# Performance work log

Measured on AMD Instinct MI355X. Metric: run time of the kernel, lower is better.

Reference implementation:

```python
import jax, jax.numpy as jnp
import numpy as np

N = 50000    # nodes
E = 800000   # edges (avg degree 16)
IN = 256     # in_dim
HID = 256    # hidden_dim
OUT = 128    # out_dim


def setup_inputs() -> dict:
    key = jax.random.key(0)
    ks = jax.random.split(key, 9)
    features = jax.random.normal(ks[0], (N, IN), jnp.float32)
    src = jax.random.randint(ks[1], (E,), 0, N, jnp.int32)
    dst = jax.random.randint(ks[2], (E,), 0, N, jnp.int32)
    noise = jax.random.normal(ks[3], (N, OUT), jnp.float32)
    def glorot(k, shape, fan):
        return jax.random.normal(k, shape, jnp.float32) / np.float32(np.sqrt(fan))
    W1 = glorot(ks[4], (IN, HID), IN);  b1 = jnp.zeros((HID,), jnp.float32)
    W2 = glorot(ks[5], (HID, OUT), HID); b2 = jnp.zeros((OUT,), jnp.float32)
    W3 = glorot(ks[6], (HID, OUT), HID); b3 = jnp.zeros((OUT,), jnp.float32)
    fcW = glorot(ks[7], (HID, IN), IN)   # nn.Linear(in_dim, hidden_dim).weight: [HID, IN]
    return dict(features=features, noise=noise, W1=W1, b1=b1, W2=W2, b2=b2,
                W3=W3, b3=b3, fcW=fcW, src=src, dst=dst)


def _gcn(x, W, b, src, dst, out_norm, in_norm):
    """DGL GraphConv norm='both': D_out^{-1/2} A D_in^{-1/2} X W + b."""
    x = x * out_norm[:, None]          # scale src features by out-deg^{-1/2}
    x = x @ W                          # dense transform (order commutes with SpMM)
    agg = jax.ops.segment_sum(x[src], dst, num_segments=N)  # sparse aggregate
    return agg * in_norm[:, None] + b


def reference(features, noise, W1, b1, W2, b2, W3, b3, fcW, src, dst):
    ones = jnp.ones((E,), jnp.float32)
    out_deg = jax.ops.segment_sum(ones, src, num_segments=N)
    in_deg = jax.ops.segment_sum(ones, dst, num_segments=N)
    out_norm = jnp.maximum(out_deg, 1.0) ** -0.5
    in_norm = jnp.maximum(in_deg, 1.0) ** -0.5

    h = jax.nn.relu(_gcn(features, W1, b1, src, dst, out_norm, in_norm))
    mean = jax.nn.relu(_gcn(h, W2, b2, src, dst, out_norm, in_norm))
    log_std = _gcn(h, W3, b3, src, dst, out_norm, in_norm)  # identity activation
    z = mean + noise * jnp.exp(log_std)
    seq_fts = features @ fcW.T
    return z, h, seq_fts
```

## Files before the change

kernel.cpp:

```cpp
#include <hip/hip_runtime.h>
#include <hip/hip_bf16.h>
#include <stdint.h>
#include <math.h>

#define IN_DIM 256
#define HID_DIM 256
#define OUT_DIM 128

typedef __attribute__((ext_vector_type(8))) short short8;
typedef __attribute__((ext_vector_type(4))) float floatx4;

__device__ __forceinline__ float bf2f(ushort u) {
  union { uint32_t i; float f; } v; v.i = ((uint32_t)u) << 16; return v.f;
}
__device__ __forceinline__ ushort f2bf(float f) {
  union { float f; uint32_t u; } v; v.f = f;
  uint32_t u = v.u;
  uint32_t r = u + 0x7fffu + ((u >> 16) & 1u);
  return (ushort)(r >> 16);
}

__global__ void f2b_kernel(const float* __restrict__ in, ushort* __restrict__ out, int n) {
  int base = (blockIdx.x * 256 + threadIdx.x) * 4;
  if (base < n) {
    float4 v = *(const float4*)(in + base);
    ushort4 o;
    o.x = f2bf(v.x); o.y = f2bf(v.y); o.z = f2bf(v.z); o.w = f2bf(v.w);
    *(ushort4*)(out + base) = o;
  }
}

__global__ void deg_kernel(const int* __restrict__ src, const int* __restrict__ dst,
                           int* __restrict__ out_deg, int* __restrict__ in_deg, int E) {
  int e = blockIdx.x * 256 + threadIdx.x;
  if (e < E) {
    atomicAdd(&out_deg[src[e]], 1);
    atomicAdd(&in_deg[dst[e]], 1);
  }
}

__global__ void scan_sums(const int* __restrict__ deg, int* __restrict__ chunk_sum, int n) {
  __shared__ int lds[256];
  int b = blockIdx.x, t = threadIdx.x;
  int base = b * 1024 + t * 4;
  int s = 0;
  if (base + 3 < n) {
    int4 v = *(const int4*)(deg + base);
    s = v.x + v.y + v.z + v.w;
  } else {
    for (int i = 0; i < 4; ++i) if (base + i < n) s += deg[base + i];
  }
  lds[t] = s;
  __syncthreads();
  for (int off = 128; off > 0; off >>= 1) {
    if (t < off) lds[t] += lds[t + off];
    __syncthreads();
  }
  if (t == 0) chunk_sum[b] = lds[0];
}

__global__ void scan_chunks(const int* __restrict__ chunk_sum, int* __restrict__ chunk_off,
                            int nchunks, int* __restrict__ row_ptr) {
  __shared__ int lds[256];
  int t = threadIdx.x;
  int v = (t < nchunks) ? chunk_sum[t] : 0;
  lds[t] = v;
  __syncthreads();
  for (int off = 1; off < 256; off <<= 1) {
    int add = (t >= off) ? lds[t - off] : 0;
    __syncthreads();
    lds[t] += add;
    __syncthreads();
  }
  if (t < nchunks) chunk_off[t] = lds[t] - v;
  if (t == 0) row_ptr[0] = 0;
}

__global__ void scan_final(const int* __restrict__ deg, const int* __restrict__ chunk_off,
                           int* __restrict__ row_ptr, int n) {
  __shared__ int lds[256];
  int b = blockIdx.x, t = threadIdx.x;
  int base = b * 1024 + t * 4;
  int v[4]; int s = 0;
#pragma unroll
  for (int i = 0; i < 4; ++i) { v[i] = (base + i < n) ? deg[base + i] : 0; s += v[i]; }
  lds[t] = s;
  __syncthreads();
  for (int off = 1; off < 256; off <<= 1) {
    int add = (t >= off) ? lds[t - off] : 0;
    __syncthreads();
    lds[t] += add;
    __syncthreads();
  }
  int run = lds[t] - s + chunk_off[b];
#pragma unroll
  for (int i = 0; i < 4; ++i) {
    run += v[i];
    if (base + i < n) row_ptr[base + i + 1] = run;
  }
}

__global__ void fill_kernel(const int* __restrict__ src, const int* __restrict__ dst,
                            const int* __restrict__ row_ptr, int* __restrict__ fill_cnt,
                            const int* __restrict__ out_deg,
                            int* __restrict__ edge_src, float* __restrict__ edge_w, int E) {
  int e = blockIdx.x * 256 + threadIdx.x;
  if (e < E) {
    int d = dst[e];
    int s = src[e];
    int pos = row_ptr[d] + atomicAdd(&fill_cnt[d], 1);
    int od = out_deg[s]; if (od < 1) od = 1;
    edge_src[pos] = s;
    edge_w[pos] = rsqrtf((float)od);
  }
}

__global__ void prep_weights(const float* __restrict__ W1, const float* __restrict__ W2,
                             const float* __restrict__ W3, const float* __restrict__ b2,
                             const float* __restrict__ b3, const float* __restrict__ fcW,
                             ushort* __restrict__ W1T, ushort* __restrict__ WcT,
                             float* __restrict__ bcat, ushort* __restrict__ fcWb) {
  int k = blockIdx.x;
  int n = threadIdx.x;
  W1T[n * 256 + k] = f2bf(W1[k * 256 + n]);
  WcT[n * 256 + k] = f2bf((n < 128) ? W2[k * 128 + n] : W3[k * 128 + (n - 128)]);
  fcWb[k * 256 + n] = f2bf(fcW[k * 256 + n]);
  if (k == 0) bcat[n] = (n < 128) ? b2[n] : b3[n - 128];
}

__global__ __launch_bounds__(256) void agg_kernel(
    const ushort* __restrict__ x, const int* __restrict__ row_ptr,
    const int* __restrict__ edge_src, const float* __restrict__ edge_w,
    const int* __restrict__ in_deg, ushort* __restrict__ out, int N) {
  int wave = threadIdx.x >> 6, lane = threadIdx.x & 63;
  int n = blockIdx.x * 4 + wave;
  if (n >= N) return;
  int half = lane >> 5;
  int hl = lane & 31;
  int start = row_ptr[n], end = row_ptr[n + 1];
  float acc[8];
#pragma unroll
  for (int k = 0; k < 8; ++k) acc[k] = 0.f;

  for (int base = start; base < end; base += 4) {
    int i0 = base + half;
    int i1 = base + 2 + half;
    int s0 = 0, s1 = 0; float w0 = 0.f, w1 = 0.f;
    if (i0 < end) { s0 = edge_src[i0]; w0 = edge_w[i0]; }
    if (i1 < end) { s1 = edge_src[i1]; w1 = edge_w[i1]; }
    uint4 v0 = *(const uint4*)&x[(size_t)s0 * 256 + hl * 8];
    uint4 v1 = *(const uint4*)&x[(size_t)s1 * 256 + hl * 8];
    const uint32_t* p0 = (const uint32_t*)&v0;
    const uint32_t* p1 = (const uint32_t*)&v1;
#pragma unroll
    for (int k = 0; k < 4; ++k) {
      acc[2 * k]     += bf2f((ushort)(p0[k] & 0xffffu)) * w0;
      acc[2 * k + 1] += bf2f((ushort)(p0[k] >> 16)) * w0;
      acc[2 * k]     += bf2f((ushort)(p1[k] & 0xffffu)) * w1;
      acc[2 * k + 1] += bf2f((ushort)(p1[k] >> 16)) * w1;
    }
  }
#pragma unroll
  for (int k = 0; k < 8; ++k) acc[k] += __shfl_xor(acc[k], 32, 64);

  if (half == 0) {
    int id = in_deg[n]; if (id < 1) id = 1;
    float inn = rsqrtf((float)id);
    uint4 o;
    uint32_t* po = (uint32_t*)&o;
#pragma unroll
    for (int k = 0; k < 4; ++k) {
      po[k] = ((uint32_t)f2bf(acc[2 * k + 1] * inn) << 16) |
              (uint32_t)f2bf(acc[2 * k] * inn);
    }
    *(uint4*)&out[(size_t)n * 256 + hl * 8] = o;
  }
}

__global__ __launch_bounds__(256, 2) void gemm_kernel(
    const ushort* __restrict__ A, const ushort* __restrict__ BT,
    const float* __restrict__ bias, const float* __restrict__ noise,
    float* __restrict__ C32, ushort* __restrict__ Cbf, int M, int mode) {
  __shared__ alignas(16) ushort A_lds[128 * 72];
  __shared__ alignas(16) ushort B_lds[256 * 72];
  int t = threadIdx.x;
  int m0 = blockIdx.x * 128;
  int wave = t >> 6, lane = t & 63;
  int wm = wave * 32;
  int l15 = lane & 15, quad = lane >> 4;

  floatx4 acc[2][16];
#pragma unroll
  for (int i = 0; i < 2; ++i)
#pragma unroll
    for (int j = 0; j < 16; ++j) acc[i][j] = (floatx4)(0.f);

  for (int kc = 0; kc < 256; kc += 64) {
#pragma unroll
    for (int r = 0; r < 4; ++r) {
      int idx = t + r * 256;
      int row = idx >> 3;
      int c = (idx & 7) << 3;
      int grow = m0 + row; if (grow > M - 1) grow = M - 1;
      *(uint4*)&A_lds[row * 72 + c] = *(const uint4*)(A + (size_t)grow * 256 + kc + c);
    }
#pragma unroll
    for (int r = 0; r < 8; ++r) {
      int idx = t + r * 256;
      int row = idx >> 3;
      int c = (idx & 7) << 3;
      *(uint4*)&B_lds[row * 72 + c] = *(const uint4*)(BT + (size_t)row * 256 + kc + c);
    }
    __syncthreads();
#pragma unroll
    for (int ko = 0; ko < 2; ++ko) {
      short8 a[2];
#pragma unroll
      for (int i = 0; i < 2; ++i)
        a[i] = *(const short8*)&A_lds[(wm + i * 16 + l15) * 72 + ko * 32 + quad * 8];
#pragma unroll
      for (int j = 0; j < 16; ++j) {
        short8 b = *(const short8*)&B_lds[(j * 16 + l15) * 72 + ko * 32 + quad * 8];
#pragma unroll
        for (int i = 0; i < 2; ++i)
          acc[i][j] = __builtin_amdgcn_mfma_f32_16x16x32_bf16(a[i], b, acc[i][j], 0, 0, 0);
      }
    }
    __syncthreads();
  }

  if (mode == 1) {
#pragma unroll
    for (int i = 0; i < 2; ++i) {
#pragma unroll
      for (int j = 0; j < 8; ++j) {
        int col = j * 16 + l15;
        float bm = bias[col];
        float bl = bias[col + 128];
#pragma unroll
        for (int r = 0; r < 4; ++r) {
          int row = m0 + wm + i * 16 + quad * 4 + r;
          if (row < M) {
            float mean = acc[i][j][r] + bm;
            float ls = acc[i][j + 8][r] + bl;
            size_t o = (size_t)row * 128 + col;
            C32[o] = fmaxf(mean, 0.f) + noise[o] * expf(ls);
          }
        }
      }
    }
  } else {
#pragma unroll
    for (int i = 0; i < 2; ++i) {
#pragma unroll
      for (int j = 0; j < 16; ++j) {
        int col = j * 16 + l15;
        float bv = (mode == 0) ? bias[col] : 0.f;
#pragma unroll
        for (int r = 0; r < 4; ++r) {
          int row = m0 + wm + i * 16 + quad * 4 + r;
          if (row < M) {
            float v = acc[i][j][r] + bv;
            if (mode == 0) v = fmaxf(v, 0.f);
            size_t o = (size_t)row * 256 + col;
            C32[o] = v;
            if (mode == 0) Cbf[o] = f2bf(v);
          }
        }
      }
    }
  }
}

extern "C" void kernel_launch(void* const* d_in, const int* in_sizes, int n_in,
                              void* d_out, int out_size, void* d_ws, size_t ws_size,
                              hipStream_t stream) {
  const float* features = (const float*)d_in[0];
  const float* noise    = (const float*)d_in[1];
  const float* W1 = (const float*)d_in[2];
  const float* b1 = (const float*)d_in[3];
  const float* W2 = (const float*)d_in[4];
  const float* b2 = (const float*)d_in[5];
  const float* W3 = (const float*)d_in[6];
  const float* b3 = (const float*)d_in[7];
  const float* fcW = (const float*)d_in[8];
  const int* src = (const int*)d_in[9];
  const int* dst = (const int*)d_in[10];
  const int N = in_sizes[0] / IN_DIM;
  const int E = in_sizes[9];

  float* out = (float*)d_out;
  float* z_out = out;
  float* h_out = out + (size_t)N * OUT_DIM;
  float* s_out = h_out + (size_t)N * HID_DIM;

  char* w = (char*)d_ws;
  auto carve = [&](size_t bytes) {
    char* p = w;
    w += (bytes + 255) & ~(size_t)255;
    return p;
  };
  ushort* feat_bf = (ushort*)carve((size_t)N * 256 * 2);
  ushort* h_bf    = (ushort*)carve((size_t)N * 256 * 2);
  ushort* agg_buf = (ushort*)carve((size_t)N * 256 * 2);
  ushort* W1T  = (ushort*)carve(256 * 256 * 2);
  ushort* WcT  = (ushort*)carve(256 * 256 * 2);
  ushort* fcWb = (ushort*)carve(256 * 256 * 2);
  float*  bcat = (float*)carve(256 * 4);
  int* degs    = (int*)carve((size_t)3 * N * 4);
  int* out_deg = degs;
  int* in_deg  = degs + N;
  int* fill_cnt = degs + 2 * N;
  int* row_ptr  = (int*)carve((size_t)(N + 1) * 4);
  int* edge_src = (int*)carve((size_t)E * 4);
  float* edge_w = (float*)carve((size_t)E * 4);
  int* chunk_sum = (int*)carve(256 * 4);
  int* chunk_off = (int*)carve(256 * 4);

  const int nchunks = (N + 1023) / 1024;

  hipMemsetAsync(degs, 0, (size_t)3 * N * 4, stream);
  deg_kernel<<<(E + 255) / 256, 256, 0, stream>>>(src, dst, out_deg, in_deg, E);
  scan_sums<<<nchunks, 256, 0, stream>>>(in_deg, chunk_sum, N);
  scan_chunks<<<1, 256, 0, stream>>>(chunk_sum, chunk_off, nchunks, row_ptr);
  scan_final<<<nchunks, 256, 0, stream>>>(in_deg, chunk_off, row_ptr, N);
  fill_kernel<<<(E + 255) / 256, 256, 0, stream>>>(src, dst, row_ptr, fill_cnt, out_deg,
                                                   edge_src, edge_w, E);

  f2b_kernel<<<((N * 256 / 4) + 255) / 256, 256, 0, stream>>>(features, feat_bf, N * 256);
  prep_weights<<<256, 256, 0, stream>>>(W1, W2, W3, b2, b3, fcW, W1T, WcT, bcat, fcWb);

  int gblocks = (N + 127) / 128;
  agg_kernel<<<(N + 3) / 4, 256, 0, stream>>>(feat_bf, row_ptr, edge_src, edge_w, in_deg, agg_buf, N);
  gemm_kernel<<<gblocks, 256, 0, stream>>>(agg_buf, W1T, b1, (const float*)nullptr,
                                           h_out, h_bf, N, 0);
  agg_kernel<<<(N + 3) / 4, 256, 0, stream>>>(h_bf, row_ptr, edge_src, edge_w, in_deg, agg_buf, N);
  gemm_kernel<<<gblocks, 256, 0, stream>>>(agg_buf, WcT, bcat, noise,
                                           z_out, (ushort*)nullptr, N, 1);
  gemm_kernel<<<gblocks, 256, 0, stream>>>(feat_bf, fcWb, (const float*)nullptr,
                                           (const float*)nullptr, s_out, (ushort*)nullptr, N, 2);
}
```

Measured before the change: 558.2 us.

## Fuse feature bf16 conversion into seq GEMM, pack edge records, prefetch agg indices

The standalone fp32-to-bf16 feature conversion kernel is removed. The seq_fts GEMM (mode 2) now reads fp32 features directly, converts them in registers, and writes the bf16 copy for the first aggregation to use. Edge source and weight are packed into one int2 array so each edge needs one 8-byte load. The aggregation loop now processes 8 edges per iteration and software-prefetches the next batch of edge records to hide index-load latency. The cost is more register pressure in agg and a wider fp32 A load in the mode-2 GEMM. There is also a grow-clamp duplicate write to the bf16 buffer on the tail block, which is benign.

```diff
diff --git a/kernel.cpp b/kernel.cpp
--- a/kernel.cpp
+++ b/kernel.cpp
@@ -18,16 +18,6 @@
   uint32_t u = v.u;
   uint32_t r = u + 0x7fffu + ((u >> 16) & 1u);
   return (ushort)(r >> 16);
-}
-
-__global__ void f2b_kernel(const float* __restrict__ in, ushort* __restrict__ out, int n) {
-  int base = (blockIdx.x * 256 + threadIdx.x) * 4;
-  if (base < n) {
-    float4 v = *(const float4*)(in + base);
-    ushort4 o;
-    o.x = f2bf(v.x); o.y = f2bf(v.y); o.z = f2bf(v.z); o.w = f2bf(v.w);
-    *(ushort4*)(out + base) = o;
-  }
 }
 
 __global__ void deg_kernel(const int* __restrict__ src, const int* __restrict__ dst,
@@ -103,15 +93,17 @@
 __global__ void fill_kernel(const int* __restrict__ src, const int* __restrict__ dst,
                             const int* __restrict__ row_ptr, int* __restrict__ fill_cnt,
                             const int* __restrict__ out_deg,
-                            int* __restrict__ edge_src, float* __restrict__ edge_w, int E) {
+                            int2* __restrict__ edge_sw, int E) {
   int e = blockIdx.x * 256 + threadIdx.x;
   if (e < E) {
     int d = dst[e];
     int s = src[e];
     int pos = row_ptr[d] + atomicAdd(&fill_cnt[d], 1);
     int od = out_deg[s]; if (od < 1) od = 1;
-    edge_src[pos] = s;
-    edge_w[pos] = rsqrtf((float)od);
+    int2 rec;
+    rec.x = s;
+    rec.y = __float_as_int(rsqrtf((float)od));
+    edge_sw[pos] = rec;
   }
 }
 
@@ -130,7 +122,7 @@
 
 __global__ __launch_bounds__(256) void agg_kernel(
     const ushort* __restrict__ x, const int* __restrict__ row_ptr,
-    const int* __restrict__ edge_src, const float* __restrict__ edge_w,
+    const int2* __restrict__ edge_sw,
     const int* __restrict__ in_deg, ushort* __restrict__ out, int N) {
   int wave = threadIdx.x >> 6, lane = threadIdx.x & 63;
   int n = blockIdx.x * 4 + wave;
@@ -138,47 +130,67 @@
   int half = lane >> 5;
   int hl = lane & 31;
   int start = row_ptr[n], end = row_ptr[n + 1];
+  int id = in_deg[n]; if (id < 1) id = 1;
+  float inn = rsqrtf((float)id);
+
   float acc[8];
 #pragma unroll
   for (int k = 0; k < 8; ++k) acc[k] = 0.f;
 
-  for (int base = start; base < end; base += 4) {
-    int i0 = base + half;
-    int i1 = base + 2 + half;
-    int s0 = 0, s1 = 0; float w0 = 0.f, w1 = 0.f;
-    if (i0 < end) { s0 = edge_src[i0]; w0 = edge_w[i0]; }
-    if (i1 < end) { s1 = edge_src[i1]; w1 = edge_w[i1]; }
-    uint4 v0 = *(const uint4*)&x[(size_t)s0 * 256 + hl * 8];
-    uint4 v1 = *(const uint4*)&x[(size_t)s1 * 256 + hl * 8];
-    const uint32_t* p0 = (const uint32_t*)&v0;
-    const uint32_t* p1 = (const uint32_t*)&v1;
+  int cs[4]; float cw[4];
+#pragma unroll
+  for (int k = 0; k < 4; ++k) {
+    int i = start + half + 2 * k;
+    cs[k] = 0; cw[k] = 0.f;
+    if (i < end) { int2 e = edge_sw[i]; cs[k] = e.x; cw[k] = __int_as_float(e.y); }
+  }
+
+  for (int base = start; base < end; base += 8) {
+    uint4 v[4];
+#pragma unroll
+    for (int k = 0; k < 4; ++k)
+      v[k] = *(const uint4*)&x[(size_t)cs[k] * 256 + hl * 8];
+
+    int ns[4]; float nw[4];
 #pragma unroll
     for (int k = 0; k < 4; ++k) {
-      acc[2 * k]     += bf2f((ushort)(p0[k] & 0xffffu)) * w0;
-      acc[2 * k + 1] += bf2f((ushort)(p0[k] >> 16)) * w0;
-      acc[2 * k]     += bf2f((ushort)(p1[k] & 0xffffu)) * w1;
-      acc[2 * k + 1] += bf2f((ushort)(p1[k] >> 16)) * w1;
-    }
-  }
+      int i = base + 8 + half + 2 * k;
+      ns[k] = 0; nw[k] = 0.f;
+      if (i < end) { int2 e = edge_sw[i]; ns[k] = e.x; nw[k] = __int_as_float(e.y); }
+    }
+
+#pragma unroll
+    for (int k = 0; k < 4; ++k) {
+      const uint32_t* p = (const uint32_t*)&v[k];
+      float wk = cw[k];
+#pragma unroll
+      for (int q = 0; q < 4; ++q) {
+        acc[2 * q]     += bf2f((ushort)(p[q] & 0xffffu)) * wk;
+        acc[2 * q + 1] += bf2f((ushort)(p[q] >> 16)) * wk;
+      }
+    }
+#pragma unroll
+    for (int k = 0; k < 4; ++k) { cs[k] = ns[k]; cw[k] = nw[k]; }
+  }
+
 #pragma unroll
   for (int k = 0; k < 8; ++k) acc[k] += __shfl_xor(acc[k], 32, 64);
 
   if (half == 0) {
-    int id = in_deg[n]; if (id < 1) id = 1;
-    float inn = rsqrtf((float)id);
     uint4 o;
     uint32_t* po = (uint32_t*)&o;
 #pragma unroll
-    for (int k = 0; k < 4; ++k) {
-      po[k] = ((uint32_t)f2bf(acc[2 * k + 1] * inn) << 16) |
-              (uint32_t)f2bf(acc[2 * k] * inn);
+    for (int q = 0; q < 4; ++q) {
+      po[q] = ((uint32_t)f2bf(acc[2 * q + 1] * inn) << 16) |
+              (uint32_t)f2bf(acc[2 * q] * inn);
     }
     *(uint4*)&out[(size_t)n * 256 + hl * 8] = o;
   }
 }
 
 __global__ __launch_bounds__(256, 2) void gemm_kernel(
-    const ushort* __restrict__ A, const ushort* __restrict__ BT,
+    const ushort* __restrict__ A, const float* __restrict__ A32,
+    const ushort* __restrict__ BT,
     const float* __restrict__ bias, const float* __restrict__ noise,
     float* __restrict__ C32, ushort* __restrict__ Cbf, int M, int mode) {
   __shared__ alignas(16) ushort A_lds[128 * 72];
@@ -196,13 +208,28 @@
     for (int j = 0; j < 16; ++j) acc[i][j] = (floatx4)(0.f);
 
   for (int kc = 0; kc < 256; kc += 64) {
-#pragma unroll
-    for (int r = 0; r < 4; ++r) {
-      int idx = t + r * 256;
-      int row = idx >> 3;
-      int c = (idx & 7) << 3;
-      int grow = m0 + row; if (grow > M - 1) grow = M - 1;
-      *(uint4*)&A_lds[row * 72 + c] = *(const uint4*)(A + (size_t)grow * 256 + kc + c);
+    if (mode == 2) {
+#pragma unroll
+      for (int r = 0; r < 8; ++r) {
+        int idx = t + r * 256;
+        int row = idx >> 4;
+        int c = (idx & 15) << 2;
+        int grow = m0 + row; if (grow > M - 1) grow = M - 1;
+        float4 v = *(const float4*)(A32 + (size_t)grow * 256 + kc + c);
+        ushort4 o;
+        o.x = f2bf(v.x); o.y = f2bf(v.y); o.z = f2bf(v.z); o.w = f2bf(v.w);
+        *(ushort4*)&A_lds[row * 72 + c] = o;
+        *(ushort4*)(Cbf + (size_t)grow * 256 + kc + c) = o;
+      }
+    } else {
+#pragma unroll
+      for (int r = 0; r < 4; ++r) {
+        int idx = t + r * 256;
+        int row = idx >> 3;
+        int c = (idx & 7) << 3;
+        int grow = m0 + row; if (grow > M - 1) grow = M - 1;
+        *(uint4*)&A_lds[row * 72 + c] = *(const uint4*)(A + (size_t)grow * 256 + kc + c);
+      }
     }
 #pragma unroll
     for (int r = 0; r < 8; ++r) {
@@ -312,8 +339,7 @@
   int* in_deg  = degs + N;
   int* fill_cnt = degs + 2 * N;
   int* row_ptr  = (int*)carve((size_t)(N + 1) * 4);
-  int* edge_src = (int*)carve((size_t)E * 4);
-  float* edge_w = (float*)carve((size_t)E * 4);
+  int2* edge_sw = (int2*)carve((size_t)E * 8);
   int* chunk_sum = (int*)carve(256 * 4);
   int* chunk_off = (int*)carve(256 * 4);
 
@@ -325,18 +351,18 @@
   scan_chunks<<<1, 256, 0, stream>>>(chunk_sum, chunk_off, nchunks, row_ptr);
   scan_final<<<nchunks, 256, 0, stream>>>(in_deg, chunk_off, row_ptr, N);
   fill_kernel<<<(E + 255) / 256, 256, 0, stream>>>(src, dst, row_ptr, fill_cnt, out_deg,
-                                                   edge_src, edge_w, E);
-
-  f2b_kernel<<<((N * 256 / 4) + 255) / 256, 256, 0, stream>>>(features, feat_bf, N * 256);
+                                                   edge_sw, E);
+
   prep_weights<<<256, 256, 0, stream>>>(W1, W2, W3, b2, b3, fcW, W1T, WcT, bcat, fcWb);
 
   int gblocks = (N + 127) / 128;
-  agg_kernel<<<(N + 3) / 4, 256, 0, stream>>>(feat_bf, row_ptr, edge_src, edge_w, in_deg, agg_buf, N);
-  gemm_kernel<<<gblocks, 256, 0, stream>>>(agg_buf, W1T, b1, (const float*)nullptr,
-                                           h_out, h_bf, N, 0);
-  agg_kernel<<<(N + 3) / 4, 256, 0, stream>>>(h_bf, row_ptr, edge_src, edge_w, in_deg, agg_buf, N);
-  gemm_kernel<<<gblocks, 256, 0, stream>>>(agg_buf, WcT, bcat, noise,
-                                           z_out, (ushort*)nullptr, N, 1);
-  gemm_kernel<<<gblocks, 256, 0, stream>>>(feat_bf, fcWb, (const float*)nullptr,
-                                           (const float*)nullptr, s_out, (ushort*)nullptr, N, 2);
-}
+  gemm_kernel<<<gblocks, 256, 0, stream>>>((const ushort*)nullptr, features, fcWb,
+                                           (const float*)nullptr, (const float*)nullptr,
+                                           s_out, feat_bf, N, 2);
+  agg_kernel<<<(N + 3) / 4, 256, 0, stream>>>(feat_bf, row_ptr, edge_sw, in_deg, agg_buf, N);
+  gemm_kernel<<<gblocks, 256, 0, stream>>>(agg_buf, (const float*)nullptr, W1T, b1,
+                                           (const float*)nullptr, h_out, h_bf, N, 0);
+  agg_kernel<<<(N + 3) / 4, 256, 0, stream>>>(h_bf, row_ptr, edge_sw, in_deg, agg_buf, N);
+  gemm_kernel<<<gblocks, 256, 0, stream>>>(agg_buf, (const float*)nullptr, WcT, bcat,
+                                           noise, z_out, (ushort*)nullptr, N, 1);
+}
```

Result: faster. 537.6 us (-3.7%).
